# Kernel optimization log

Hardware: AMD Instinct MI355X
Metric: run time of the kernel (lower is better)

Reference implementation:

```python
import jax, jax.numpy as jnp
import numpy as np

SIM_THRESHOLD = 0.7
EPS = 1e-8  # matches torch F.cosine_similarity eps

Q, M, D, C = 4096, 65536, 384, 128


def setup_inputs() -> dict:
    key = jax.random.key(0)
    k1, k2, k3 = jax.random.split(key, 3)
    query_embeddings = jax.random.normal(k1, (Q, D), dtype=jnp.float32)
    memory_embeddings = jax.random.normal(k2, (M, D), dtype=jnp.float32)
    # per-example one-hot-ish label vectors [M, C]
    memory_labels = jax.random.uniform(k3, (M, C), dtype=jnp.float32)
    return {
        "query_embeddings": query_embeddings,
        "memory_embeddings": memory_embeddings,
        "memory_labels": memory_labels,
    }


def _l2_normalize(x):
    n = jnp.sqrt(jnp.sum(x * x, axis=-1, keepdims=True))
    return x / jnp.maximum(n, EPS)


def reference(query_embeddings, memory_embeddings, memory_labels):
    # cosine similarity matrix [Q, M] via normalized GEMM
    qn = _l2_normalize(query_embeddings)          # [Q, D]
    mn = _l2_normalize(memory_embeddings)         # [M, D]
    sims = jnp.einsum("qd,md->qm", qn, mn)        # [Q, M]
    max_sim = jnp.max(sims, axis=1)               # [Q]
    max_idx = jnp.argmax(sims, axis=1)            # [Q]
    picked = memory_labels[max_idx]               # [Q, C] gather
    C_ = memory_labels.shape[1]
    uniform = jnp.full((1, C_), 1.0 / C_, dtype=picked.dtype)
    predictions = jnp.where((max_sim > SIM_THRESHOLD)[:, None], picked, uniform)
    return predictions
```

## Files before the change

### kernel.cpp

```cpp
#include <hip/hip_runtime.h>
#include <math.h>

#define QN 4096
#define MN 65536
#define DN 384
#define CN 128
#define NCHUNK 64
#define MROWS_PER_CHUNK (MN / NCHUNK)
#define MT_PER (MROWS_PER_CHUNK / 64)
#define BTILE_B (64 * DN)

typedef __attribute__((ext_vector_type(8))) int i32x8;
typedef __attribute__((ext_vector_type(4))) int i32x4;
typedef __attribute__((ext_vector_type(4))) float f32x4;

__device__ __forceinline__ unsigned char f2fp8(float f) {
  return (unsigned char)(__builtin_amdgcn_cvt_pk_fp8_f32(f, 0.f, 0, false) & 0xff);
}

__device__ __forceinline__ void async16(const void* g, void* l) {
  __builtin_amdgcn_global_load_lds(
      (const __attribute__((address_space(1))) unsigned int*)g,
      (__attribute__((address_space(3))) unsigned int*)l, 16, 0, 0);
}

__global__ __launch_bounds__(256) void nrm_kernel(const float* __restrict__ qe,
                                                  const float* __restrict__ me,
                                                  unsigned char* __restrict__ yq,
                                                  unsigned char* __restrict__ ym) {
  const int row = blockIdx.x * 4 + (threadIdx.x >> 6);
  const int lane = threadIdx.x & 63;
  const float* xr;
  unsigned char* yr;
  if (row < QN) {
    xr = qe + (size_t)row * DN;
    yr = yq + (size_t)row * DN;
  } else {
    xr = me + (size_t)(row - QN) * DN;
    yr = ym + (size_t)(row - QN) * DN;
  }
  float v[6];
  float ss = 0.f;
#pragma unroll
  for (int i = 0; i < 6; ++i) {
    v[i] = xr[lane + i * 64];
    ss += v[i] * v[i];
  }
#pragma unroll
  for (int m = 1; m < 64; m <<= 1) ss += __shfl_xor(ss, m);
  const float scale = 1.0f / fmaxf(sqrtf(ss), 1e-8f);
#pragma unroll
  for (int i = 0; i < 6; ++i) yr[lane + i * 64] = f2fp8(v[i] * scale);
}

__global__ __launch_bounds__(256, 2) void gemm_max_kernel(
    const unsigned char* __restrict__ qn8, const unsigned char* __restrict__ mn8,
    float* __restrict__ pmax) {
  __shared__ unsigned char Bs[2 * BTILE_B];
  __shared__ float smax[2][128];

  const int tid = threadIdx.x;
  const int wave = tid >> 6, lane = tid & 63;
  const int wr = wave >> 1, wc = wave & 1;
  const int quad = lane >> 4, l16 = lane & 15;
  const int r7 = l16 & 7;
  const int qrow0 = blockIdx.x * 128;
  const int mchunk0 = blockIdx.y * MROWS_PER_CHUNK;

  float rmax[16];
#pragma unroll
  for (int i = 0; i < 16; ++i) rmax[i] = -3.0e38f;

  {
    const unsigned char* abase = qn8 + (size_t)qrow0 * DN;
#pragma unroll
    for (int i = 0; i < 12; ++i) {
      const int ci = i * 256 + tid;
      const int row = ci / 24;
      const int j = ci - row * 24;
      const int gj = (j & 24) | ((j ^ row) & 7);
      async16(abase + row * DN + gj * 16, &Bs[(i * 256 + wave * 64) * 16]);
    }
  }
  __syncthreads();
  i32x8 afr[3][4];
#pragma unroll
  for (int kc = 0; kc < 3; ++kc)
#pragma unroll
    for (int rt = 0; rt < 4; ++rt) {
      const unsigned char* p = &Bs[(wr * 64 + rt * 16 + l16) * DN];
      i32x4 lo = *(const i32x4*)&p[(kc * 8 + ((quad * 2 + 0) ^ r7)) * 16];
      i32x4 hi = *(const i32x4*)&p[(kc * 8 + ((quad * 2 + 1) ^ r7)) * 16];
      afr[kc][rt][0] = lo[0]; afr[kc][rt][1] = lo[1];
      afr[kc][rt][2] = lo[2]; afr[kc][rt][3] = lo[3];
      afr[kc][rt][4] = hi[0]; afr[kc][rt][5] = hi[1];
      afr[kc][rt][6] = hi[2]; afr[kc][rt][7] = hi[3];
    }
  __syncthreads();

  int srcoff[6];
#pragma unroll
  for (int i = 0; i < 6; ++i) {
    const int ci = i * 256 + tid;
    const int row = ci / 24;
    const int j = ci - row * 24;
    const int gj = (j & 24) | ((j ^ row) & 7);
    srcoff[i] = row * DN + gj * 16;
  }

  const unsigned char* bchunk = mn8 + (size_t)mchunk0 * DN;
#pragma unroll
  for (int i = 0; i < 6; ++i)
    async16(bchunk + srcoff[i], &Bs[(i * 256 + wave * 64) * 16]);

#pragma unroll 1
  for (int mt = 0; mt < MT_PER; ++mt) {
    __syncthreads();
    unsigned char* cur = &Bs[(mt & 1) * BTILE_B];
    if (mt + 1 < MT_PER) {
      unsigned char* nxt = &Bs[((mt + 1) & 1) * BTILE_B];
      const unsigned char* nb = bchunk + (size_t)(mt + 1) * BTILE_B;
#pragma unroll
      for (int i = 0; i < 6; ++i)
        async16(nb + srcoff[i], &nxt[(i * 256 + wave * 64) * 16]);
    }

    f32x4 acc[4][2];
#pragma unroll
    for (int rt = 0; rt < 4; ++rt)
#pragma unroll
      for (int ct = 0; ct < 2; ++ct) acc[rt][ct] = (f32x4){0.f, 0.f, 0.f, 0.f};

#pragma unroll
    for (int kc = 0; kc < 3; ++kc) {
      i32x8 bfr[2];
#pragma unroll
      for (int ct = 0; ct < 2; ++ct) {
        const unsigned char* p = &cur[(wc * 32 + ct * 16 + l16) * DN];
        i32x4 lo = *(const i32x4*)&p[(kc * 8 + ((quad * 2 + 0) ^ r7)) * 16];
        i32x4 hi = *(const i32x4*)&p[(kc * 8 + ((quad * 2 + 1) ^ r7)) * 16];
        bfr[ct][0] = lo[0]; bfr[ct][1] = lo[1];
        bfr[ct][2] = lo[2]; bfr[ct][3] = lo[3];
        bfr[ct][4] = hi[0]; bfr[ct][5] = hi[1];
        bfr[ct][6] = hi[2]; bfr[ct][7] = hi[3];
      }
#pragma unroll
      for (int rt = 0; rt < 4; ++rt)
#pragma unroll
        for (int ct = 0; ct < 2; ++ct)
          acc[rt][ct] = __builtin_amdgcn_mfma_scale_f32_16x16x128_f8f6f4(
              afr[kc][rt], bfr[ct], acc[rt][ct], 0, 0,
              0, 0x7f7f7f7f, 0, 0x7f7f7f7f);
    }

#pragma unroll
    for (int rt = 0; rt < 4; ++rt)
#pragma unroll
      for (int r = 0; r < 4; ++r) {
        const float v = fmaxf(acc[rt][0][r], acc[rt][1][r]);
        rmax[rt * 4 + r] = fmaxf(rmax[rt * 4 + r], v);
      }
  }

#pragma unroll
  for (int i = 0; i < 16; ++i) {
    float v = rmax[i];
    v = fmaxf(v, __shfl_xor(v, 1));
    v = fmaxf(v, __shfl_xor(v, 2));
    v = fmaxf(v, __shfl_xor(v, 4));
    v = fmaxf(v, __shfl_xor(v, 8));
    rmax[i] = v;
  }
  if (l16 == 0) {
#pragma unroll
    for (int rt = 0; rt < 4; ++rt)
#pragma unroll
      for (int r = 0; r < 4; ++r)
        smax[wc][wr * 64 + rt * 16 + quad * 4 + r] = rmax[rt * 4 + r];
  }
  __syncthreads();
  if (tid < 128) {
    const float v = fmaxf(smax[0][tid], smax[1][tid]);
    pmax[(size_t)(qrow0 + tid) * NCHUNK + blockIdx.y] = v;
  }
}

__global__ __launch_bounds__(256) void decide_kernel(
    const float* __restrict__ pmax, const float* __restrict__ qe,
    const float* __restrict__ me, const float* __restrict__ labels,
    float* __restrict__ out) {
  const int q = blockIdx.x;
  const int t = threadIdx.x;
  __shared__ float smx;
  if (t < 64) {
    float v = pmax[(size_t)q * NCHUNK + t];
#pragma unroll
    for (int m = 1; m < 64; m <<= 1) v = fmaxf(v, __shfl_xor(v, m));
    if (t == 0) smx = v;
  }
  __syncthreads();
  if (smx <= 0.5f) {
    if (t < CN) out[(size_t)q * CN + t] = 1.0f / 128.0f;
    return;
  }
  __shared__ float sred[256];
  __shared__ int sidx[256];
  __shared__ float wsum[4];
  const float* qr = qe + (size_t)q * DN;
  float ss = 0.f;
  for (int i = t; i < DN; i += 256) ss += qr[i] * qr[i];
#pragma unroll
  for (int m = 1; m < 64; m <<= 1) ss += __shfl_xor(ss, m);
  if ((t & 63) == 0) wsum[t >> 6] = ss;
  __syncthreads();
  const float qnorm = fmaxf(sqrtf(wsum[0] + wsum[1] + wsum[2] + wsum[3]), 1e-8f);

  float best = -3.0e38f;
  int bidx = 0x7fffffff;
  for (int j = t; j < MN; j += 256) {
    const float* mr = me + (size_t)j * DN;
    float dot = 0.f, ms = 0.f;
    for (int k = 0; k < DN; ++k) {
      float a = qr[k], b = mr[k];
      dot += a * b;
      ms += b * b;
    }
    const float sim = dot / (qnorm * fmaxf(sqrtf(ms), 1e-8f));
    if (sim > best) { best = sim; bidx = j; }
  }
  sred[t] = best;
  sidx[t] = bidx;
  __syncthreads();
  for (int s = 128; s > 0; s >>= 1) {
    if (t < s) {
      const float ov = sred[t + s];
      const int oi = sidx[t + s];
      if (ov > sred[t] || (ov == sred[t] && oi < sidx[t])) {
        sred[t] = ov;
        sidx[t] = oi;
      }
    }
    __syncthreads();
  }
  const float mx = sred[0];
  const int mi = sidx[0];
  if (t < CN)
    out[(size_t)q * CN + t] =
        (mx > 0.7f) ? labels[(size_t)mi * CN + t] : (1.0f / 128.0f);
}

extern "C" void kernel_launch(void* const* d_in, const int* in_sizes, int n_in,
                              void* d_out, int out_size, void* d_ws,
                              size_t ws_size, hipStream_t stream) {
  const float* qe = (const float*)d_in[0];
  const float* me = (const float*)d_in[1];
  const float* lb = (const float*)d_in[2];
  float* out = (float*)d_out;

  char* ws = (char*)d_ws;
  const size_t OFF_QN = 0;
  const size_t OFF_MN = OFF_QN + (size_t)QN * DN;
  const size_t OFF_PMAX = OFF_MN + (size_t)MN * DN;
  unsigned char* qn8 = (unsigned char*)(ws + OFF_QN);
  unsigned char* mn8 = (unsigned char*)(ws + OFF_MN);
  float* pmax = (float*)(ws + OFF_PMAX);

  nrm_kernel<<<(QN + MN) / 4, 256, 0, stream>>>(qe, me, qn8, mn8);
  gemm_max_kernel<<<dim3(QN / 128, NCHUNK), 256, 0, stream>>>(qn8, mn8, pmax);
  decide_kernel<<<QN, 256, 0, stream>>>(pmax, qe, me, lb, out);
}
```

Before: 254.5 us.

## Pre-swizzle memory fp8 into MFMA fragment layout and load B directly to registers

The normalize kernel now writes memory embeddings in a tiled layout that matches the MFMA B-fragment order. The GEMM kernel then loads B fragments straight from global memory into registers with a software-pipelined double buffer, instead of staging them through LDS. This removes the LDS double buffer and the per-iteration barriers. In exchange each wave issues its own global loads, so the loop depends on L2/global latency being hidden by the prefetch depth; LDS is now used only for the A tile.

```diff
diff --git a/kernel.cpp b/kernel.cpp
--- a/kernel.cpp
+++ b/kernel.cpp
@@ -8,11 +8,14 @@
 #define NCHUNK 64
 #define MROWS_PER_CHUNK (MN / NCHUNK)
 #define MT_PER (MROWS_PER_CHUNK / 64)
-#define BTILE_B (64 * DN)
+#define TILE_B 6144
+#define MT_B (4 * TILE_B)
 
 typedef __attribute__((ext_vector_type(8))) int i32x8;
 typedef __attribute__((ext_vector_type(4))) int i32x4;
 typedef __attribute__((ext_vector_type(4))) float f32x4;
+
+union frag8 { i32x4 h[2]; i32x8 v8; };
 
 __device__ __forceinline__ unsigned char f2fp8(float f) {
   return (unsigned char)(__builtin_amdgcn_cvt_pk_fp8_f32(f, 0.f, 0, false) & 0xff);
@@ -22,6 +25,24 @@
   __builtin_amdgcn_global_load_lds(
       (const __attribute__((address_space(1))) unsigned int*)g,
       (__attribute__((address_space(3))) unsigned int*)l, 16, 0, 0);
+}
+
+__device__ __forceinline__ void pf2(frag8* d, const unsigned char* p) {
+  d[0].h[0] = *(const i32x4*)(p);
+  d[0].h[1] = *(const i32x4*)(p + 256);
+  d[1].h[0] = *(const i32x4*)(p + TILE_B);
+  d[1].h[1] = *(const i32x4*)(p + TILE_B + 256);
+}
+
+__device__ __forceinline__ void mfma8(const i32x8 (&a)[4], const frag8 (&b)[2],
+                                      f32x4 (&acc)[4][2]) {
+#pragma unroll
+  for (int rt = 0; rt < 4; ++rt)
+#pragma unroll
+    for (int ct = 0; ct < 2; ++ct)
+      acc[rt][ct] = __builtin_amdgcn_mfma_scale_f32_16x16x128_f8f6f4(
+          a[rt], b[ct].v8, acc[rt][ct], 0, 0,
+          0, 0x7f7f7f7f, 0, 0x7f7f7f7f);
 }
 
 __global__ __launch_bounds__(256) void nrm_kernel(const float* __restrict__ qe,
@@ -30,15 +51,8 @@
                                                   unsigned char* __restrict__ ym) {
   const int row = blockIdx.x * 4 + (threadIdx.x >> 6);
   const int lane = threadIdx.x & 63;
-  const float* xr;
-  unsigned char* yr;
-  if (row < QN) {
-    xr = qe + (size_t)row * DN;
-    yr = yq + (size_t)row * DN;
-  } else {
-    xr = me + (size_t)(row - QN) * DN;
-    yr = ym + (size_t)(row - QN) * DN;
-  }
+  const float* xr = (row < QN) ? qe + (size_t)row * DN
+                               : me + (size_t)(row - QN) * DN;
   float v[6];
   float ss = 0.f;
 #pragma unroll
@@ -49,14 +63,25 @@
 #pragma unroll
   for (int m = 1; m < 64; m <<= 1) ss += __shfl_xor(ss, m);
   const float scale = 1.0f / fmaxf(sqrtf(ss), 1e-8f);
-#pragma unroll
-  for (int i = 0; i < 6; ++i) yr[lane + i * 64] = f2fp8(v[i] * scale);
+  if (row < QN) {
+    unsigned char* yr = yq + (size_t)row * DN;
+#pragma unroll
+    for (int i = 0; i < 6; ++i) yr[lane + i * 64] = f2fp8(v[i] * scale);
+  } else {
+    const int r = row - QN;
+    unsigned char* tb = ym + (size_t)(r >> 4) * TILE_B + (r & 15) * 16;
+#pragma unroll
+    for (int i = 0; i < 6; ++i) {
+      const int p = lane + i * 64;
+      tb[(p >> 4) * 256 + (p & 15)] = f2fp8(v[i] * scale);
+    }
+  }
 }
 
 __global__ __launch_bounds__(256, 2) void gemm_max_kernel(
-    const unsigned char* __restrict__ qn8, const unsigned char* __restrict__ mn8,
+    const unsigned char* __restrict__ qn8, const unsigned char* __restrict__ mn8f,
     float* __restrict__ pmax) {
-  __shared__ unsigned char Bs[2 * BTILE_B];
+  __shared__ unsigned char As[128 * DN];
   __shared__ float smax[2][128];
 
   const int tid = threadIdx.x;
@@ -79,7 +104,7 @@
       const int row = ci / 24;
       const int j = ci - row * 24;
       const int gj = (j & 24) | ((j ^ row) & 7);
-      async16(abase + row * DN + gj * 16, &Bs[(i * 256 + wave * 64) * 16]);
+      async16(abase + row * DN + gj * 16, &As[(i * 256 + wave * 64) * 16]);
     }
   }
   __syncthreads();
@@ -88,7 +113,7 @@
   for (int kc = 0; kc < 3; ++kc)
 #pragma unroll
     for (int rt = 0; rt < 4; ++rt) {
-      const unsigned char* p = &Bs[(wr * 64 + rt * 16 + l16) * DN];
+      const unsigned char* p = &As[(wr * 64 + rt * 16 + l16) * DN];
       i32x4 lo = *(const i32x4*)&p[(kc * 8 + ((quad * 2 + 0) ^ r7)) * 16];
       i32x4 hi = *(const i32x4*)&p[(kc * 8 + ((quad * 2 + 1) ^ r7)) * 16];
       afr[kc][rt][0] = lo[0]; afr[kc][rt][1] = lo[1];
@@ -96,70 +121,52 @@
       afr[kc][rt][4] = hi[0]; afr[kc][rt][5] = hi[1];
       afr[kc][rt][6] = hi[2]; afr[kc][rt][7] = hi[3];
     }
-  __syncthreads();
-
-  int srcoff[6];
-#pragma unroll
-  for (int i = 0; i < 6; ++i) {
-    const int ci = i * 256 + tid;
-    const int row = ci / 24;
-    const int j = ci - row * 24;
-    const int gj = (j & 24) | ((j ^ row) & 7);
-    srcoff[i] = row * DN + gj * 16;
-  }
-
-  const unsigned char* bchunk = mn8 + (size_t)mchunk0 * DN;
-#pragma unroll
-  for (int i = 0; i < 6; ++i)
-    async16(bchunk + srcoff[i], &Bs[(i * 256 + wave * 64) * 16]);
+
+  const unsigned char* bp = mn8f + (size_t)((mchunk0 + wc * 32) >> 4) * TILE_B +
+                            (quad * 2) * 256 + l16 * 16;
+  frag8 bfr[2][2];
+  pf2(bfr[0], bp);
 
 #pragma unroll 1
-  for (int mt = 0; mt < MT_PER; ++mt) {
-    __syncthreads();
-    unsigned char* cur = &Bs[(mt & 1) * BTILE_B];
-    if (mt + 1 < MT_PER) {
-      unsigned char* nxt = &Bs[((mt + 1) & 1) * BTILE_B];
-      const unsigned char* nb = bchunk + (size_t)(mt + 1) * BTILE_B;
-#pragma unroll
-      for (int i = 0; i < 6; ++i)
-        async16(nb + srcoff[i], &nxt[(i * 256 + wave * 64) * 16]);
-    }
+  for (int mt2 = 0; mt2 < MT_PER / 2; ++mt2) {
+    const unsigned char* p0 = bp + (size_t)(2 * mt2) * MT_B;
+    const unsigned char* p1 = p0 + MT_B;
+    const unsigned char* p2 = (2 * mt2 + 2 < MT_PER) ? p1 + MT_B : bp;
 
     f32x4 acc[4][2];
 #pragma unroll
     for (int rt = 0; rt < 4; ++rt)
 #pragma unroll
       for (int ct = 0; ct < 2; ++ct) acc[rt][ct] = (f32x4){0.f, 0.f, 0.f, 0.f};
-
-#pragma unroll
-    for (int kc = 0; kc < 3; ++kc) {
-      i32x8 bfr[2];
-#pragma unroll
-      for (int ct = 0; ct < 2; ++ct) {
-        const unsigned char* p = &cur[(wc * 32 + ct * 16 + l16) * DN];
-        i32x4 lo = *(const i32x4*)&p[(kc * 8 + ((quad * 2 + 0) ^ r7)) * 16];
-        i32x4 hi = *(const i32x4*)&p[(kc * 8 + ((quad * 2 + 1) ^ r7)) * 16];
-        bfr[ct][0] = lo[0]; bfr[ct][1] = lo[1];
-        bfr[ct][2] = lo[2]; bfr[ct][3] = lo[3];
-        bfr[ct][4] = hi[0]; bfr[ct][5] = hi[1];
-        bfr[ct][6] = hi[2]; bfr[ct][7] = hi[3];
-      }
-#pragma unroll
-      for (int rt = 0; rt < 4; ++rt)
-#pragma unroll
-        for (int ct = 0; ct < 2; ++ct)
-          acc[rt][ct] = __builtin_amdgcn_mfma_scale_f32_16x16x128_f8f6f4(
-              afr[kc][rt], bfr[ct], acc[rt][ct], 0, 0,
-              0, 0x7f7f7f7f, 0, 0x7f7f7f7f);
-    }
-
-#pragma unroll
-    for (int rt = 0; rt < 4; ++rt)
-#pragma unroll
-      for (int r = 0; r < 4; ++r) {
-        const float v = fmaxf(acc[rt][0][r], acc[rt][1][r]);
-        rmax[rt * 4 + r] = fmaxf(rmax[rt * 4 + r], v);
-      }
+    pf2(bfr[1], p0 + 2048);
+    mfma8(afr[0], bfr[0], acc);
+    pf2(bfr[0], p0 + 4096);
+    mfma8(afr[1], bfr[1], acc);
+    pf2(bfr[1], p1);
+    mfma8(afr[2], bfr[0], acc);
+#pragma unroll
+    for (int rt = 0; rt < 4; ++rt)
+#pragma unroll
+      for (int r = 0; r < 4; ++r)
+        rmax[rt * 4 + r] =
+            fmaxf(rmax[rt * 4 + r], fmaxf(acc[rt][0][r], acc[rt][1][r]));
+
+#pragma unroll
+    for (int rt = 0; rt < 4; ++rt)
+#pragma unroll
+      for (int ct = 0; ct < 2; ++ct) acc[rt][ct] = (f32x4){0.f, 0.f, 0.f, 0.f};
+    pf2(bfr[0], p1 + 2048);
+    mfma8(afr[0], bfr[1], acc);
+    pf2(bfr[1], p1 + 4096);
+    mfma8(afr[1], bfr[0], acc);
+    pf2(bfr[0], p2);
+    mfma8(afr[2], bfr[1], acc);
+#pragma unroll
+    for (int rt = 0; rt < 4; ++rt)
+#pragma unroll
+      for (int r = 0; r < 4; ++r)
+        rmax[rt * 4 + r] =
+            fmaxf(rmax[rt * 4 + r], fmaxf(acc[rt][0][r], acc[rt][1][r]));
   }
 
 #pragma unroll
@@ -171,6 +178,7 @@
     v = fmaxf(v, __shfl_xor(v, 8));
     rmax[i] = v;
   }
+  __syncthreads();
   if (l16 == 0) {
 #pragma unroll
     for (int rt = 0; rt < 4; ++rt)
@@ -262,10 +270,10 @@
   const size_t OFF_MN = OFF_QN + (size_t)QN * DN;
   const size_t OFF_PMAX = OFF_MN + (size_t)MN * DN;
   unsigned char* qn8 = (unsigned char*)(ws + OFF_QN);
-  unsigned char* mn8 = (unsigned char*)(ws + OFF_MN);
+  unsigned char* mn8f = (unsigned char*)(ws + OFF_MN);
   float* pmax = (float*)(ws + OFF_PMAX);
 
-  nrm_kernel<<<(QN + MN) / 4, 256, 0, stream>>>(qe, me, qn8, mn8);
-  gemm_max_kernel<<<dim3(QN / 128, NCHUNK), 256, 0, stream>>>(qn8, mn8, pmax);
+  nrm_kernel<<<(QN + MN) / 4, 256, 0, stream>>>(qe, me, qn8, mn8f);
+  gemm_max_kernel<<<dim3(QN / 128, NCHUNK), 256, 0, stream>>>(qn8, mn8f, pmax);
   decide_kernel<<<QN, 256, 0, stream>>>(pmax, qe, me, lb, out);
 }
```

After: 281.4 us. 1.11x slower.
